# Performance work log

Hardware: AMD Instinct MI355X
Metric: run time of the kernel (lower is better)

The kernel has to match this reference:

```python
import jax, jax.numpy as jnp
import numpy as np

N_NODES = 50000
N_EDGES = 800000
N_GRAPHS = 512
F_IN = 128
D = 256
EPS = 1e-5
NEG_SLOPE = 0.01  # torch LeakyReLU default


def leaky_relu(x):
    return jnp.where(x >= 0, x, NEG_SLOPE * x)


def egnn_conv(x, edge_index, edge_attr, lin2_w, lin2_b, lin_w, lin_b, n_nodes):
    # message: LeakyReLU(lin(x_j + lin2(edge_attr))), aggregate: add at target i
    src, dst = edge_index[0], edge_index[1]
    ea = edge_attr @ lin2_w.T + lin2_b          # [E, in]
    msg = (x[src] + ea) @ lin_w.T + lin_b        # [E, out]
    msg = leaky_relu(msg)
    return jax.ops.segment_sum(msg, dst, num_segments=n_nodes)


def batch_norm(x, w, b):
    # training-mode BatchNorm1d: biased batch statistics over node axis
    mean = jnp.mean(x, axis=0)
    var = jnp.mean(jnp.square(x - mean), axis=0)
    return (x - mean) * jax.lax.rsqrt(var + EPS) * w + b


def setup_inputs() -> dict:
    key = jax.random.key(0)
    ks = jax.random.split(key, 8)
    inp = {
        "node_ids": jax.random.randint(ks[0], (N_NODES,), 0, 51),
        "edge_index": jax.random.randint(ks[1], (2, N_EDGES), 0, N_NODES),
        "edge_attr": jax.random.normal(ks[2], (N_EDGES, 4), dtype=jnp.float32),
        "batch": jnp.sort(jax.random.randint(ks[3], (N_NODES,), 0, N_GRAPHS)),
        "emb_table": jax.random.normal(ks[4], (51, F_IN), dtype=jnp.float32) * 0.1,
        "c1_lin2_w": jax.random.normal(ks[5], (F_IN, 4), dtype=jnp.float32) * 0.1,
        "c1_lin2_b": jnp.zeros((F_IN,), jnp.float32),
        "c1_lin_w": jax.random.normal(ks[6], (D, F_IN), dtype=jnp.float32) * (1.0 / np.sqrt(F_IN)),
        "c1_lin_b": jnp.zeros((D,), jnp.float32),
        "bn1_w": jnp.ones((D,), jnp.float32),
        "bn1_b": jnp.zeros((D,), jnp.float32),
        "c2_lin2_w": jax.random.normal(jax.random.fold_in(key, 10), (D, 4), dtype=jnp.float32) * 0.1,
        "c2_lin2_b": jnp.zeros((D,), jnp.float32),
        "c2_lin_w": jax.random.normal(ks[7], (D, D), dtype=jnp.float32) * (1.0 / np.sqrt(D)),
        "c2_lin_b": jnp.zeros((D,), jnp.float32),
        "bn2_w": jnp.ones((D,), jnp.float32),
        "bn2_b": jnp.zeros((D,), jnp.float32),
        "gate_w": jax.random.normal(jax.random.fold_in(key, 11), (1, D), dtype=jnp.float32) * 0.1,
        "gate_b": jnp.zeros((1,), jnp.float32),
    }
    return inp


def reference(node_ids, edge_index, edge_attr, batch, emb_table,
              c1_lin2_w, c1_lin2_b, c1_lin_w, c1_lin_b, bn1_w, bn1_b,
              c2_lin2_w, c2_lin2_b, c2_lin_w, c2_lin_b, bn2_w, bn2_b,
              gate_w, gate_b):
    x = emb_table[node_ids]                                   # [N, F_IN]
    x = egnn_conv(x, edge_index, edge_attr, c1_lin2_w, c1_lin2_b,
                  c1_lin_w, c1_lin_b, N_NODES)                # [N, D]
    x = leaky_relu(batch_norm(x, bn1_w, bn1_b))
    x2 = egnn_conv(x, edge_index, edge_attr, c2_lin2_w, c2_lin2_b,
                   c2_lin_w, c2_lin_b, N_NODES)               # [N, D]
    x2 = leaky_relu(batch_norm(x2, bn2_w, bn2_b))
    # AttentionalAggregation: softmax of gate over each graph segment
    gate = x2 @ gate_w.T + gate_b                             # [N, 1]
    gmax = jax.ops.segment_max(gate, batch, num_segments=N_GRAPHS)
    e = jnp.exp(gate - gmax[batch])                           # [N, 1]
    denom = jax.ops.segment_sum(e, batch, num_segments=N_GRAPHS)
    alpha = e / denom[batch]
    out = jax.ops.segment_sum(alpha * x2, batch, num_segments=N_GRAPHS)
    return out                                                # [G, D]
```

## Files before the change

kernel.cpp:

```cpp
#include <hip/hip_runtime.h>
#include <hip/hip_bf16.h>

#define NN 50000
#define NE 800000
#define NG 512

typedef __bf16 bf16_t;
typedef __bf16 bf16x8 __attribute__((ext_vector_type(8)));
typedef __bf16 bf16x4 __attribute__((ext_vector_type(4)));
typedef float f32x4 __attribute__((ext_vector_type(4)));
typedef float f32x2 __attribute__((ext_vector_type(2)));

__device__ __forceinline__ float lrelu(float v) { return v >= 0.f ? v : 0.01f * v; }

__device__ __forceinline__ f32x2 unpk2(unsigned w) {
    union { unsigned u; float f; } lo, hi;
    lo.u = w << 16;
    hi.u = w & 0xffff0000u;
    f32x2 r; r[0] = lo.f; r[1] = hi.f; return r;
}

__device__ __forceinline__ int vzero() {
    int vz;
    asm("v_mov_b32 %0, 0" : "=v"(vz));
    return vz;
}

__global__ void gme_setup(const float* __restrict__ emb,
                          const float* __restrict__ c1lw, const float* __restrict__ c1l2w,
                          const float* __restrict__ c1l2b, const float* __restrict__ c1lb,
                          const float* __restrict__ c2lw, const float* __restrict__ c2l2w,
                          const float* __restrict__ c2l2b, const float* __restrict__ c2lb,
                          bf16_t* __restrict__ TYB, float* __restrict__ WC1,
                          float* __restrict__ WC2, float* __restrict__ CB2,
                          bf16_t* __restrict__ W2B, int* __restrict__ CNT) {
    int b = blockIdx.x, t = threadIdx.x;
    if (b < 51) {
        const float4* er = (const float4*)(emb + b * 128);
        const float4* zb = (const float4*)c1l2b;
        const float4* wr = (const float4*)(c1lw + t * 128);
        float s = 0.f;
        for (int k = 0; k < 32; ++k) {
            float4 e = er[k], z = zb[k], w = wr[k];
            s += (e.x + z.x) * w.x + (e.y + z.y) * w.y + (e.z + z.z) * w.z + (e.w + z.w) * w.w;
        }
        TYB[b * 256 + t] = (bf16_t)(s + c1lb[t]);
    } else if (b == 51) {
        const float4* wr = (const float4*)(c1lw + t * 128);
        const float4* cw = (const float4*)c1l2w;
        float4 a = make_float4(0.f, 0.f, 0.f, 0.f);
        for (int k = 0; k < 32; ++k) {
            float4 w = wr[k];
            float4 c0 = cw[k * 4 + 0], c1 = cw[k * 4 + 1], c2 = cw[k * 4 + 2], c3 = cw[k * 4 + 3];
            a.x += w.x * c0.x + w.y * c1.x + w.z * c2.x + w.w * c3.x;
            a.y += w.x * c0.y + w.y * c1.y + w.z * c2.y + w.w * c3.y;
            a.z += w.x * c0.z + w.y * c1.z + w.z * c2.z + w.w * c3.z;
            a.w += w.x * c0.w + w.y * c1.w + w.z * c2.w + w.w * c3.w;
        }
        ((float4*)WC1)[t] = a;
    } else if (b == 52) {
        const float4* wr = (const float4*)(c2lw + t * 256);
        const float4* cw = (const float4*)c2l2w;
        const float4* zb = (const float4*)c2l2b;
        float4 a = make_float4(0.f, 0.f, 0.f, 0.f);
        float ab = 0.f;
        for (int k = 0; k < 64; ++k) {
            float4 w = wr[k];
            float4 c0 = cw[k * 4 + 0], c1 = cw[k * 4 + 1], c2 = cw[k * 4 + 2], c3 = cw[k * 4 + 3];
            float4 z = zb[k];
            a.x += w.x * c0.x + w.y * c1.x + w.z * c2.x + w.w * c3.x;
            a.y += w.x * c0.y + w.y * c1.y + w.z * c2.y + w.w * c3.y;
            a.z += w.x * c0.z + w.y * c1.z + w.z * c2.z + w.w * c3.z;
            a.w += w.x * c0.w + w.y * c1.w + w.z * c2.w + w.w * c3.w;
            ab += w.x * z.x + w.y * z.y + w.z * z.z + w.w * z.w;
        }
        ((float4*)WC2)[t] = a;
        CB2[t] = ab + c2lb[t];
    } else if (b < 117) {
        int i0 = (b - 53) * 1024;
        for (int r = 0; r < 4; ++r) {
            int i = i0 + r * 256 + t;
            W2B[i] = (bf16_t)c2lw[i];
        }
    } else {
        int i = (b - 117) * 256 + t;
        if (i < NN) CNT[i] = 0;
    }
}

__global__ void gme_count(const int* __restrict__ ei, int* __restrict__ cnt,
                          int* __restrict__ RK) {
    int e = blockIdx.x * 256 + threadIdx.x;
    if (e >= NE) return;
    RK[e] = atomicAdd(&cnt[ei[NE + e]], 1);
}

__global__ void gme_scan1(const int* __restrict__ CNT, int* __restrict__ LP,
                          int* __restrict__ BS) {
    __shared__ int lds[256];
    int b = blockIdx.x, t = threadIdx.x;
    int i = b * 196 + t;
    int v = (t < 196 && i < NN) ? CNT[i] : 0;
    lds[t] = v;
    __syncthreads();
    for (int off = 1; off < 256; off <<= 1) {
        int u = (t >= off) ? lds[t - off] : 0;
        __syncthreads();
        lds[t] += u;
        __syncthreads();
    }
    if (t < 196 && i < NN) LP[i] = lds[t] - v;
    if (t == 255) BS[b] = lds[255];
}

__global__ void gme_scan2(const int* __restrict__ BS, int* __restrict__ BX,
                          int* __restrict__ RS) {
    __shared__ int lds[256];
    int t = threadIdx.x;
    int v = BS[t];
    lds[t] = v;
    __syncthreads();
    for (int off = 1; off < 256; off <<= 1) {
        int u = (t >= off) ? lds[t - off] : 0;
        __syncthreads();
        lds[t] += u;
        __syncthreads();
    }
    BX[t] = lds[t] - v;
    if (t == 255) RS[NN] = lds[255];
}

__global__ void gme_scan3(const int* __restrict__ LP, const int* __restrict__ BX,
                          int* __restrict__ RS,
                          const int* __restrict__ batch, int* __restrict__ GS) {
    int b = blockIdx.x, t = threadIdx.x;
    if (t >= 196) return;
    int i = b * 196 + t;
    if (i >= NN) return;
    RS[i] = BX[b] + LP[i];
    int bb = batch[i];
    if (i == 0) {
        for (int g = 0; g <= bb; ++g) GS[g] = 0;
    } else {
        int a = batch[i - 1];
        for (int g = a + 1; g <= bb; ++g) GS[g] = i;
    }
    if (i == NN - 1) {
        for (int g = bb + 1; g <= NG; ++g) GS[g] = NN;
    }
}

__global__ void gme_scatter(const int* __restrict__ ei,
                            const float4* __restrict__ eattr,
                            const int* __restrict__ node_ids,
                            const int* __restrict__ RS, const int* __restrict__ RK,
                            uint4* __restrict__ SE) {
    int e = blockIdx.x * 256 + threadIdx.x;
    if (e >= NE) return;
    int s = ei[e];
    int d = ei[NE + e];
    int nid = node_ids[s];
    float4 at = eattr[e];
    union { bf16_t h[2]; unsigned u; } p01, p23;
    p01.h[0] = (bf16_t)at.x; p01.h[1] = (bf16_t)at.y;
    p23.h[0] = (bf16_t)at.z; p23.h[1] = (bf16_t)at.w;
    int pos = RS[d] + RK[e];
    SE[pos] = make_uint4((unsigned)(s | (nid << 16)), p01.u, p23.u, 0u);
}

__global__ __launch_bounds__(256) void gme_conv0(
        const int* __restrict__ RS, const uint4* __restrict__ SE,
        const bf16_t* __restrict__ TYB, const float* __restrict__ Wc,
        float* __restrict__ agg, float* __restrict__ PARTS) {
    __shared__ __align__(16) uint2 sTY[51 * 64];
    {
        const uint4* s4 = (const uint4*)TYB;
        uint4* d4 = (uint4*)sTY;
        for (int i = threadIdx.x; i < 51 * 32; i += 256) d4[i] = s4[i];
    }
    __syncthreads();
    int lane = threadIdx.x & 63;
    int w = threadIdx.x >> 6;
    int vz = vzero();
    const float4* wc4 = (const float4*)Wc;
    int c4 = lane * 4;
    float4 w0 = wc4[c4 + 0], w1 = wc4[c4 + 1], w2 = wc4[c4 + 2], w3 = wc4[c4 + 3];
    f32x2 wA0 = {w0.x, w1.x}, wB0 = {w0.y, w1.y}, wC0 = {w0.z, w1.z}, wD0 = {w0.w, w1.w};
    f32x2 wA1 = {w2.x, w3.x}, wB1 = {w2.y, w3.y}, wC1 = {w2.z, w3.z}, wD1 = {w2.w, w3.w};
    const f32x2 zero = {0.f, 0.f};
    const uint2* lrow = sTY + lane;
    int base = blockIdx.x * 16 + w * 4;
    f32x2 ssum0 = zero, ssum1 = zero, qsum0 = zero, qsum1 = zero;
#pragma unroll 1
    for (int k = 0; k < 4; ++k) {
        int node = __builtin_amdgcn_readfirstlane(base + k);
        int rs = RS[node], re = RS[node + 1];
        f32x2 accP0 = zero, accP1 = zero, accA0 = zero, accA1 = zero;
        auto accum = [&](uint4 se, uint2 r) {
            f32x2 y0 = unpk2(r.x), y1 = unpk2(r.y);
            f32x2 axy = unpk2(se.y), azw = unpk2(se.z);
            f32x2 ax = {axy[0], axy[0]}, ay = {axy[1], axy[1]};
            f32x2 az = {azw[0], azw[0]}, aw = {azw[1], azw[1]};
            f32x2 m0 = __builtin_elementwise_fma(ax, wA0, y0);
            f32x2 m1 = __builtin_elementwise_fma(ax, wA1, y1);
            m0 = __builtin_elementwise_fma(ay, wB0, m0);
            m1 = __builtin_elementwise_fma(ay, wB1, m1);
            m0 = __builtin_elementwise_fma(az, wC0, m0);
            m1 = __builtin_elementwise_fma(az, wC1, m1);
            m0 = __builtin_elementwise_fma(aw, wD0, m0);
            m1 = __builtin_elementwise_fma(aw, wD1, m1);
            accA0 += m0; accA1 += m1;
            accP0 += __builtin_elementwise_max(m0, zero);
            accP1 += __builtin_elementwise_max(m1, zero);
        };
        int j = rs;
        for (; j + 8 <= re; j += 8) {
            uint4 se[8]; uint2 r[8];
#pragma unroll
            for (int u = 0; u < 8; ++u) se[u] = SE[j + u + vz];
#pragma unroll
            for (int u = 0; u < 8; ++u) r[u] = lrow[(se[u].x >> 16) << 6];
#pragma unroll
            for (int u = 0; u < 8; ++u) accum(se[u], r[u]);
        }
        if (j + 4 <= re) {
            uint4 se[4]; uint2 r[4];
#pragma unroll
            for (int u = 0; u < 4; ++u) se[u] = SE[j + u + vz];
#pragma unroll
            for (int u = 0; u < 4; ++u) r[u] = lrow[(se[u].x >> 16) << 6];
#pragma unroll
            for (int u = 0; u < 4; ++u) accum(se[u], r[u]);
            j += 4;
        }
        for (; j < re; ++j) {
            uint4 se = SE[j + vz];
            accum(se, lrow[(se.x >> 16) << 6]);
        }
        const f32x2 c99 = {0.99f, 0.99f}, c01 = {0.01f, 0.01f};
        f32x2 o0 = __builtin_elementwise_fma(accP0, c99, accA0 * c01);
        f32x2 o1 = __builtin_elementwise_fma(accP1, c99, accA1 * c01);
        *((float4*)(agg + node * 256) + lane) = make_float4(o0[0], o0[1], o1[0], o1[1]);
        ssum0 += o0; ssum1 += o1;
        qsum0 += o0 * o0; qsum1 += o1 * o1;
    }
    __syncthreads();
    float* red = (float*)sTY;
    red[w * 512 + c4 + 0] = ssum0[0]; red[w * 512 + c4 + 1] = ssum0[1];
    red[w * 512 + c4 + 2] = ssum1[0]; red[w * 512 + c4 + 3] = ssum1[1];
    red[w * 512 + 256 + c4 + 0] = qsum0[0]; red[w * 512 + 256 + c4 + 1] = qsum0[1];
    red[w * 512 + 256 + c4 + 2] = qsum1[0]; red[w * 512 + 256 + c4 + 3] = qsum1[1];
    __syncthreads();
    int cc = threadIdx.x;
    float s = red[cc] + red[512 + cc] + red[1024 + cc] + red[1536 + cc];
    float q = red[256 + cc] + red[768 + cc] + red[1280 + cc] + red[1792 + cc];
    int prow = (blockIdx.x & 255) * 512;
    atomicAdd(&PARTS[prow + cc], s);
    atomicAdd(&PARTS[prow + 256 + cc], q);
}

__global__ __launch_bounds__(256, 4) void gme_conv1(
        const int* __restrict__ RS, const uint4* __restrict__ SE,
        const bf16_t* __restrict__ QB, const float* __restrict__ Wc,
        float* __restrict__ agg, float* __restrict__ PARTS) {
    __shared__ float red[2048];
    int lane = threadIdx.x & 63;
    int w = threadIdx.x >> 6;
    int node = __builtin_amdgcn_readfirstlane(blockIdx.x * 4 + w);
    const float4* wc4 = (const float4*)Wc;
    int c4 = lane * 4;
    float4 w0 = wc4[c4 + 0], w1 = wc4[c4 + 1], w2 = wc4[c4 + 2], w3 = wc4[c4 + 3];
    f32x2 wA0 = {w0.x, w1.x}, wB0 = {w0.y, w1.y}, wC0 = {w0.z, w1.z}, wD0 = {w0.w, w1.w};
    f32x2 wA1 = {w2.x, w3.x}, wB1 = {w2.y, w3.y}, wC1 = {w2.z, w3.z}, wD1 = {w2.w, w3.w};
    const f32x2 zero = {0.f, 0.f};
    f32x2 accP0 = zero, accP1 = zero, accA0 = zero, accA1 = zero;
    int rs = RS[node], re = RS[node + 1];
    const char* yb = (const char*)QB;
    unsigned loff = (unsigned)(lane << 3);
    auto rowld = [&](unsigned row) -> uint2 {
        return *(const uint2*)(yb + (row << 9) + loff);
    };
    auto accum = [&](uint4 se, uint2 r) {
        f32x2 y0 = unpk2(r.x), y1 = unpk2(r.y);
        f32x2 axy = unpk2(se.y), azw = unpk2(se.z);
        f32x2 ax = {axy[0], axy[0]}, ay = {axy[1], axy[1]};
        f32x2 az = {azw[0], azw[0]}, aw = {azw[1], azw[1]};
        f32x2 m0 = __builtin_elementwise_fma(ax, wA0, y0);
        f32x2 m1 = __builtin_elementwise_fma(ax, wA1, y1);
        m0 = __builtin_elementwise_fma(ay, wB0, m0);
        m1 = __builtin_elementwise_fma(ay, wB1, m1);
        m0 = __builtin_elementwise_fma(az, wC0, m0);
        m1 = __builtin_elementwise_fma(az, wC1, m1);
        m0 = __builtin_elementwise_fma(aw, wD0, m0);
        m1 = __builtin_elementwise_fma(aw, wD1, m1);
        accA0 += m0; accA1 += m1;
        accP0 += __builtin_elementwise_max(m0, zero);
        accP1 += __builtin_elementwise_max(m1, zero);
    };
    int j = rs;
    if (j + 8 <= re) {
        uint4 se[8];
#pragma unroll
        for (int u = 0; u < 8; ++u) se[u] = SE[j + u];
        while (true) {
            uint2 r[8];
#pragma unroll
            for (int u = 0; u < 8; ++u) r[u] = rowld(se[u].x & 0xffffu);
            bool more = (j + 16 <= re);
            uint4 seN[8];
            if (more) {
#pragma unroll
                for (int u = 0; u < 8; ++u) seN[u] = SE[j + 8 + u];
            }
#pragma unroll
            for (int u = 0; u < 8; ++u) accum(se[u], r[u]);
            j += 8;
            if (!more) break;
#pragma unroll
            for (int u = 0; u < 8; ++u) se[u] = seN[u];
        }
    }
    if (j + 4 <= re) {
        uint4 se[4]; uint2 r[4];
#pragma unroll
        for (int u = 0; u < 4; ++u) se[u] = SE[j + u];
#pragma unroll
        for (int u = 0; u < 4; ++u) r[u] = rowld(se[u].x & 0xffffu);
#pragma unroll
        for (int u = 0; u < 4; ++u) accum(se[u], r[u]);
        j += 4;
    }
    for (; j < re; ++j) {
        uint4 se = SE[j];
        accum(se, rowld(se.x & 0xffffu));
    }
    const f32x2 c99 = {0.99f, 0.99f}, c01 = {0.01f, 0.01f};
    f32x2 o0 = __builtin_elementwise_fma(accP0, c99, accA0 * c01);
    f32x2 o1 = __builtin_elementwise_fma(accP1, c99, accA1 * c01);
    *((float4*)(agg + node * 256) + lane) = make_float4(o0[0], o0[1], o1[0], o1[1]);
    red[w * 512 + c4 + 0] = o0[0]; red[w * 512 + c4 + 1] = o0[1];
    red[w * 512 + c4 + 2] = o1[0]; red[w * 512 + c4 + 3] = o1[1];
    red[w * 512 + 256 + c4 + 0] = o0[0] * o0[0];
    red[w * 512 + 256 + c4 + 1] = o0[1] * o0[1];
    red[w * 512 + 256 + c4 + 2] = o1[0] * o1[0];
    red[w * 512 + 256 + c4 + 3] = o1[1] * o1[1];
    __syncthreads();
    int cc = threadIdx.x;
    float s = red[cc] + red[512 + cc] + red[1024 + cc] + red[1536 + cc];
    float q = red[256 + cc] + red[768 + cc] + red[1280 + cc] + red[1792 + cc];
    int prow = (blockIdx.x & 255) * 512;
    atomicAdd(&PARTS[prow + cc], s);
    atomicAdd(&PARTS[prow + 256 + cc], q);
}

__global__ __launch_bounds__(512) void gme_bred(float* __restrict__ PARTS,
                                                float* __restrict__ ST, int zero) {
    int t = threadIdx.x;
    int b = blockIdx.x;
    float acc = 0.f;
#pragma unroll
    for (int r = 0; r < 16; ++r) acc += PARTS[(b * 16 + r) * 512 + t];
    atomicAdd(&ST[t], acc);
    if (zero) {
#pragma unroll
        for (int r = 0; r < 16; ++r) PARTS[(b * 16 + r) * 512 + t] = 0.f;
    }
}

__global__ __launch_bounds__(256) void gme_gemm(const float* __restrict__ P,
                                                const float* __restrict__ ST,
                                                const float* __restrict__ bw,
                                                const float* __restrict__ bb,
                                                const bf16_t* __restrict__ W2B,
                                                const float* __restrict__ CB2,
                                                bf16_t* __restrict__ QB) {
    __shared__ float s_sc[256], s_sh[256];
    __shared__ __align__(16) uint4 sB[8192];
    {
        int c = threadIdx.x;
        float mean = ST[c] * (1.f / NN);
        float var = ST[256 + c] * (1.f / NN) - mean * mean;
        float sc = bw[c] * rsqrtf(var + 1e-5f);
        s_sc[c] = sc;
        s_sh[c] = bb[c] - mean * sc;
        const uint4* w4 = (const uint4*)W2B;
#pragma unroll
        for (int it = 0; it < 32; ++it) {
            int i = it * 256 + c;
            int row = i >> 5, slot = i & 31;
            sB[(row << 5) | (slot ^ (row & 7))] = w4[i];
        }
    }
    __syncthreads();
    int lane = threadIdx.x & 63;
    int wave = blockIdx.x * 4 + (threadIdx.x >> 6);
    if (wave >= NN / 16) return;
    int m0 = wave * 16;
    int r = lane & 15, q = lane >> 4;
    int rx = r & 7;
    const float* arow = P + (m0 + r) * 256 + q * 8;
    bf16x8 a[8];
#pragma unroll
    for (int kt = 0; kt < 8; ++kt) {
        int k0 = kt * 32 + q * 8;
        float4 u0 = *(const float4*)(arow + kt * 32);
        float4 u1 = *(const float4*)(arow + kt * 32 + 4);
        bf16x8 f;
        f[0] = (bf16_t)lrelu(fmaf(u0.x, s_sc[k0 + 0], s_sh[k0 + 0]));
        f[1] = (bf16_t)lrelu(fmaf(u0.y, s_sc[k0 + 1], s_sh[k0 + 1]));
        f[2] = (bf16_t)lrelu(fmaf(u0.z, s_sc[k0 + 2], s_sh[k0 + 2]));
        f[3] = (bf16_t)lrelu(fmaf(u0.w, s_sc[k0 + 3], s_sh[k0 + 3]));
        f[4] = (bf16_t)lrelu(fmaf(u1.x, s_sc[k0 + 4], s_sh[k0 + 4]));
        f[5] = (bf16_t)lrelu(fmaf(u1.y, s_sc[k0 + 5], s_sh[k0 + 5]));
        f[6] = (bf16_t)lrelu(fmaf(u1.z, s_sc[k0 + 6], s_sh[k0 + 6]));
        f[7] = (bf16_t)lrelu(fmaf(u1.w, s_sc[k0 + 7], s_sh[k0 + 7]));
        a[kt] = f;
    }
#pragma unroll 1
    for (int g = 0; g < 2; ++g) {
        f32x4 acc[8];
#pragma unroll
        for (int n8 = 0; n8 < 8; ++n8) acc[n8] = (f32x4){0.f, 0.f, 0.f, 0.f};
#pragma unroll
        for (int kt = 0; kt < 8; ++kt) {
            int slot = (kt * 4 + q) ^ rx;
            bf16x8 bf[8];
#pragma unroll
            for (int n8 = 0; n8 < 8; ++n8) {
                int row = g * 128 + n8 * 16 + r;
                bf[n8] = *(const bf16x8*)&sB[(row << 5) | slot];
            }
#pragma unroll
            for (int n8 = 0; n8 < 8; ++n8) {
                acc[n8] = __builtin_amdgcn_mfma_f32_16x16x32_bf16(bf[n8], a[kt], acc[n8], 0, 0, 0);
            }
        }
#pragma unroll
        for (int n8 = 0; n8 < 8; ++n8) {
            int nt = g * 8 + n8;
            float4 cbv = ((const float4*)CB2)[nt * 4 + q];
            bf16x4 o;
            o[0] = (bf16_t)(acc[n8][0] + cbv.x);
            o[1] = (bf16_t)(acc[n8][1] + cbv.y);
            o[2] = (bf16_t)(acc[n8][2] + cbv.z);
            o[3] = (bf16_t)(acc[n8][3] + cbv.w);
            *(bf16x4*)(QB + (m0 + r) * 256 + nt * 16 + q * 4) = o;
        }
    }
}

__global__ __launch_bounds__(256) void gme_attn(const int* __restrict__ GS,
                                                const float* __restrict__ P,
                                                const float* __restrict__ ST,
                                                const float* __restrict__ bw,
                                                const float* __restrict__ bb,
                                                const float* __restrict__ gw,
                                                const float* __restrict__ gb,
                                                float* __restrict__ out) {
    __shared__ float gl[1024];
    __shared__ float rr[8];
    int g = blockIdx.x, t = threadIdx.x;
    int lo = GS[g], hi = GS[g + 1];
    if (lo >= hi) { out[g * 256 + t] = 0.f; return; }
    int lane = t & 63, w = t >> 6;
    {
        float4 s4 = ((const float4*)ST)[lane];
        float4 q4 = ((const float4*)(ST + 256))[lane];
        float4 w4 = ((const float4*)bw)[lane];
        float4 b4 = ((const float4*)bb)[lane];
        float4 g4 = ((const float4*)gw)[lane];
        float m0 = s4.x * (1.f / NN), m1 = s4.y * (1.f / NN);
        float m2 = s4.z * (1.f / NN), m3 = s4.w * (1.f / NN);
        float sc0 = w4.x * rsqrtf(q4.x * (1.f / NN) - m0 * m0 + 1e-5f);
        float sc1 = w4.y * rsqrtf(q4.y * (1.f / NN) - m1 * m1 + 1e-5f);
        float sc2 = w4.z * rsqrtf(q4.z * (1.f / NN) - m2 * m2 + 1e-5f);
        float sc3 = w4.w * rsqrtf(q4.w * (1.f / NN) - m3 * m3 + 1e-5f);
        float sh0 = b4.x - m0 * sc0, sh1 = b4.y - m1 * sc1;
        float sh2 = b4.z - m2 * sc2, sh3 = b4.w - m3 * sc3;
        float gb0 = gb[0];
        for (int n = lo + w; n < hi; n += 4) {
            float4 p = *(const float4*)(P + n * 256 + lane * 4);
            float d = lrelu(fmaf(p.x, sc0, sh0)) * g4.x
                    + lrelu(fmaf(p.y, sc1, sh1)) * g4.y
                    + lrelu(fmaf(p.z, sc2, sh2)) * g4.z
                    + lrelu(fmaf(p.w, sc3, sh3)) * g4.w;
#pragma unroll
            for (int off = 32; off > 0; off >>= 1) d += __shfl_xor(d, off, 64);
            if (lane == 0) gl[n - lo] = d + gb0;
        }
    }
    __syncthreads();
    int cnt = hi - lo;
    float lm = -3.0e38f;
    for (int i = t; i < cnt; i += 256) lm = fmaxf(lm, gl[i]);
#pragma unroll
    for (int off = 32; off > 0; off >>= 1) lm = fmaxf(lm, __shfl_xor(lm, off, 64));
    if (lane == 0) rr[w] = lm;
    __syncthreads();
    float mx = fmaxf(fmaxf(rr[0], rr[1]), fmaxf(rr[2], rr[3]));
    float ls = 0.f;
    for (int i = t; i < cnt; i += 256) { float e = expf(gl[i] - mx); gl[i] = e; ls += e; }
#pragma unroll
    for (int off = 32; off > 0; off >>= 1) ls += __shfl_xor(ls, off, 64);
    if (lane == 0) rr[4 + w] = ls;
    __syncthreads();
    float sinv = 1.f / (rr[4] + rr[5] + rr[6] + rr[7]);
    float mean = ST[t] * (1.f / NN);
    float var = ST[256 + t] * (1.f / NN) - mean * mean;
    float sc = bw[t] * rsqrtf(var + 1e-5f);
    float sh = bb[t] - mean * sc;
    float a0 = 0.f, a1 = 0.f, a2 = 0.f, a3 = 0.f;
    int n = lo;
    for (; n + 4 <= hi; n += 4) {
        float p0 = P[n * 256 + t], p1 = P[(n + 1) * 256 + t];
        float p2 = P[(n + 2) * 256 + t], p3 = P[(n + 3) * 256 + t];
        a0 = fmaf(gl[n - lo + 0], lrelu(fmaf(p0, sc, sh)), a0);
        a1 = fmaf(gl[n - lo + 1], lrelu(fmaf(p1, sc, sh)), a1);
        a2 = fmaf(gl[n - lo + 2], lrelu(fmaf(p2, sc, sh)), a2);
        a3 = fmaf(gl[n - lo + 3], lrelu(fmaf(p3, sc, sh)), a3);
    }
    for (; n < hi; ++n) a0 = fmaf(gl[n - lo], lrelu(fmaf(P[n * 256 + t], sc, sh)), a0);
    out[g * 256 + t] = (a0 + a1 + a2 + a3) * sinv;
}

extern "C" void kernel_launch(void* const* d_in, const int* in_sizes, int n_in,
                              void* d_out, int out_size, void* d_ws, size_t ws_size,
                              hipStream_t stream) {
    const int* node_ids = (const int*)d_in[0];
    const int* edge_index = (const int*)d_in[1];
    const float4* edge_attr = (const float4*)d_in[2];
    const int* batch = (const int*)d_in[3];
    const float* emb = (const float*)d_in[4];
    const float* c1l2w = (const float*)d_in[5];
    const float* c1l2b = (const float*)d_in[6];
    const float* c1lw = (const float*)d_in[7];
    const float* c1lb = (const float*)d_in[8];
    const float* bn1w = (const float*)d_in[9];
    const float* bn1b = (const float*)d_in[10];
    const float* c2l2w = (const float*)d_in[11];
    const float* c2l2b = (const float*)d_in[12];
    const float* c2lw = (const float*)d_in[13];
    const float* c2lb = (const float*)d_in[14];
    const float* bn2w = (const float*)d_in[15];
    const float* bn2b = (const float*)d_in[16];
    const float* gate_w = (const float*)d_in[17];
    const float* gate_b = (const float*)d_in[18];

    char* ws = (char*)d_ws;
    size_t oP = 0;
    size_t oQB = oP + 51200000;
    size_t oSE = oQB + 25600000;
    size_t oRK = oSE + 12800000;
    size_t oRS = oRK + 3200000;
    size_t oCNT = oRS + 200064;
    size_t oLP = oCNT + 200000;
    size_t oBS = oLP + 200000;
    size_t oBX = oBS + 1024;
    size_t oTY = oBX + 1024;
    size_t oWC1 = oTY + 52224;
    size_t oWC2 = oWC1 + 4096;
    size_t oCB2 = oWC2 + 4096;
    size_t oW2B = oCB2 + 1024;
    size_t oST = oW2B + 131072;
    size_t oPARTS = oST + 4096;
    size_t oGS = oPARTS + 524288;

    float* P = (float*)(ws + oP);
    bf16_t* QB = (bf16_t*)(ws + oQB);
    uint4* SE = (uint4*)(ws + oSE);
    int* RK = (int*)(ws + oRK);
    int* RS = (int*)(ws + oRS);
    int* CNT = (int*)(ws + oCNT);
    int* LP = (int*)(ws + oLP);
    int* BS = (int*)(ws + oBS);
    int* BX = (int*)(ws + oBX);
    bf16_t* TYB = (bf16_t*)(ws + oTY);
    float* WC1 = (float*)(ws + oWC1);
    float* WC2 = (float*)(ws + oWC2);
    float* CB2 = (float*)(ws + oCB2);
    bf16_t* W2B = (bf16_t*)(ws + oW2B);
    float* ST1 = (float*)(ws + oST);
    float* ST2 = ST1 + 512;
    float* PARTS = (float*)(ws + oPARTS);
    int* GS = (int*)(ws + oGS);

    hipMemsetAsync(ST1, 0, 4096 + 524288, stream);

    gme_setup<<<313, 256, 0, stream>>>(emb, c1lw, c1l2w, c1l2b, c1lb,
                                       c2lw, c2l2w, c2l2b, c2lb,
                                       TYB, WC1, WC2, CB2, W2B, CNT);
    gme_count<<<NE / 256, 256, 0, stream>>>(edge_index, CNT, RK);
    gme_scan1<<<256, 256, 0, stream>>>(CNT, LP, BS);
    gme_scan2<<<1, 256, 0, stream>>>(BS, BX, RS);
    gme_scan3<<<256, 256, 0, stream>>>(LP, BX, RS, batch, GS);
    gme_scatter<<<NE / 256, 256, 0, stream>>>(edge_index, edge_attr, node_ids,
                                              RS, RK, SE);
    gme_conv0<<<NN / 16, 256, 0, stream>>>(RS, SE, TYB, WC1, P, PARTS);
    gme_bred<<<16, 512, 0, stream>>>(PARTS, ST1, 1);
    gme_gemm<<<(NN / 16 + 3) / 4, 256, 0, stream>>>(P, ST1, bn1w, bn1b, W2B, CB2, QB);
    gme_conv1<<<NN / 4, 256, 0, stream>>>(RS, SE, QB, WC2, P, PARTS);
    gme_bred<<<16, 512, 0, stream>>>(PARTS, ST2, 0);
    gme_attn<<<NG, 256, 0, stream>>>(GS, P, ST2, bn2w, bn2b, gate_w, gate_b,
                                     (float*)d_out);
}
```

Baseline: 363.6 us.

## Store conv aggregates in bf16 and software-pipeline edge loads in conv0

The per-node aggregate buffer P written by both conv kernels is now stored as bf16 instead of fp32, and the gemm and attention kernels read and unpack bf16. This halves the traffic of the 50000x256 intermediate on write and on its subsequent reads. Batch-norm statistics are still accumulated from the fp32 values, but the normalized inputs now carry bf16 rounding. Separately, the conv0 edge loop prefetches the next 8 edge records while accumulating the current 8, to hide global load latency at the cost of extra registers.

```diff
diff --git a/kernel.cpp b/kernel.cpp
--- a/kernel.cpp
+++ b/kernel.cpp
@@ -18,6 +18,12 @@
     lo.u = w << 16;
     hi.u = w & 0xffff0000u;
     f32x2 r; r[0] = lo.f; r[1] = hi.f; return r;
+}
+
+__device__ __forceinline__ unsigned pk2(float a, float b) {
+    union { bf16_t h[2]; unsigned u; } p;
+    p.h[0] = (bf16_t)a; p.h[1] = (bf16_t)b;
+    return p.u;
 }
 
 __device__ __forceinline__ int vzero() {
@@ -161,17 +167,14 @@
     int d = ei[NE + e];
     int nid = node_ids[s];
     float4 at = eattr[e];
-    union { bf16_t h[2]; unsigned u; } p01, p23;
-    p01.h[0] = (bf16_t)at.x; p01.h[1] = (bf16_t)at.y;
-    p23.h[0] = (bf16_t)at.z; p23.h[1] = (bf16_t)at.w;
     int pos = RS[d] + RK[e];
-    SE[pos] = make_uint4((unsigned)(s | (nid << 16)), p01.u, p23.u, 0u);
+    SE[pos] = make_uint4((unsigned)(s | (nid << 16)), pk2(at.x, at.y), pk2(at.z, at.w), 0u);
 }
 
 __global__ __launch_bounds__(256) void gme_conv0(
         const int* __restrict__ RS, const uint4* __restrict__ SE,
         const bf16_t* __restrict__ TYB, const float* __restrict__ Wc,
-        float* __restrict__ agg, float* __restrict__ PARTS) {
+        bf16_t* __restrict__ agg, float* __restrict__ PARTS) {
     __shared__ __align__(16) uint2 sTY[51 * 64];
     {
         const uint4* s4 = (const uint4*)TYB;
@@ -214,14 +217,27 @@
             accP1 += __builtin_elementwise_max(m1, zero);
         };
         int j = rs;
-        for (; j + 8 <= re; j += 8) {
-            uint4 se[8]; uint2 r[8];
+        if (j + 8 <= re) {
+            uint4 se[8];
 #pragma unroll
             for (int u = 0; u < 8; ++u) se[u] = SE[j + u + vz];
-#pragma unroll
-            for (int u = 0; u < 8; ++u) r[u] = lrow[(se[u].x >> 16) << 6];
-#pragma unroll
-            for (int u = 0; u < 8; ++u) accum(se[u], r[u]);
+            while (true) {
+                uint2 r[8];
+#pragma unroll
+                for (int u = 0; u < 8; ++u) r[u] = lrow[(se[u].x >> 16) << 6];
+                bool more = (j + 16 <= re);
+                uint4 seN[8];
+                if (more) {
+#pragma unroll
+                    for (int u = 0; u < 8; ++u) seN[u] = SE[j + 8 + u + vz];
+                }
+#pragma unroll
+                for (int u = 0; u < 8; ++u) accum(se[u], r[u]);
+                j += 8;
+                if (!more) break;
+#pragma unroll
+                for (int u = 0; u < 8; ++u) se[u] = seN[u];
+            }
         }
         if (j + 4 <= re) {
             uint4 se[4]; uint2 r[4];
@@ -240,7 +256,10 @@
         const f32x2 c99 = {0.99f, 0.99f}, c01 = {0.01f, 0.01f};
         f32x2 o0 = __builtin_elementwise_fma(accP0, c99, accA0 * c01);
         f32x2 o1 = __builtin_elementwise_fma(accP1, c99, accA1 * c01);
-        *((float4*)(agg + node * 256) + lane) = make_float4(o0[0], o0[1], o1[0], o1[1]);
+        uint2 ov;
+        ov.x = pk2(o0[0], o0[1]);
+        ov.y = pk2(o1[0], o1[1]);
+        *((uint2*)(agg + node * 256) + lane) = ov;
         ssum0 += o0; ssum1 += o1;
         qsum0 += o0 * o0; qsum1 += o1 * o1;
     }
@@ -262,7 +281,7 @@
 __global__ __launch_bounds__(256, 4) void gme_conv1(
         const int* __restrict__ RS, const uint4* __restrict__ SE,
         const bf16_t* __restrict__ QB, const float* __restrict__ Wc,
-        float* __restrict__ agg, float* __restrict__ PARTS) {
+        bf16_t* __restrict__ agg, float* __restrict__ PARTS) {
     __shared__ float red[2048];
     int lane = threadIdx.x & 63;
     int w = threadIdx.x >> 6;
@@ -337,7 +356,10 @@
     const f32x2 c99 = {0.99f, 0.99f}, c01 = {0.01f, 0.01f};
     f32x2 o0 = __builtin_elementwise_fma(accP0, c99, accA0 * c01);
     f32x2 o1 = __builtin_elementwise_fma(accP1, c99, accA1 * c01);
-    *((float4*)(agg + node * 256) + lane) = make_float4(o0[0], o0[1], o1[0], o1[1]);
+    uint2 ov;
+    ov.x = pk2(o0[0], o0[1]);
+    ov.y = pk2(o1[0], o1[1]);
+    *((uint2*)(agg + node * 256) + lane) = ov;
     red[w * 512 + c4 + 0] = o0[0]; red[w * 512 + c4 + 1] = o0[1];
     red[w * 512 + c4 + 2] = o1[0]; red[w * 512 + c4 + 3] = o1[1];
     red[w * 512 + 256 + c4 + 0] = o0[0] * o0[0];
@@ -367,7 +389,7 @@
     }
 }
 
-__global__ __launch_bounds__(256) void gme_gemm(const float* __restrict__ P,
+__global__ __launch_bounds__(256) void gme_gemm(const bf16_t* __restrict__ P,
                                                 const float* __restrict__ ST,
                                                 const float* __restrict__ bw,
                                                 const float* __restrict__ bb,
@@ -398,22 +420,22 @@
     int m0 = wave * 16;
     int r = lane & 15, q = lane >> 4;
     int rx = r & 7;
-    const float* arow = P + (m0 + r) * 256 + q * 8;
+    const uint4* arow = (const uint4*)(P + (m0 + r) * 256);
     bf16x8 a[8];
 #pragma unroll
     for (int kt = 0; kt < 8; ++kt) {
         int k0 = kt * 32 + q * 8;
-        float4 u0 = *(const float4*)(arow + kt * 32);
-        float4 u1 = *(const float4*)(arow + kt * 32 + 4);
+        uint4 u = arow[q + kt * 4];
+        f32x2 v0 = unpk2(u.x), v1 = unpk2(u.y), v2 = unpk2(u.z), v3 = unpk2(u.w);
         bf16x8 f;
-        f[0] = (bf16_t)lrelu(fmaf(u0.x, s_sc[k0 + 0], s_sh[k0 + 0]));
-        f[1] = (bf16_t)lrelu(fmaf(u0.y, s_sc[k0 + 1], s_sh[k0 + 1]));
-        f[2] = (bf16_t)lrelu(fmaf(u0.z, s_sc[k0 + 2], s_sh[k0 + 2]));
-        f[3] = (bf16_t)lrelu(fmaf(u0.w, s_sc[k0 + 3], s_sh[k0 + 3]));
-        f[4] = (bf16_t)lrelu(fmaf(u1.x, s_sc[k0 + 4], s_sh[k0 + 4]));
-        f[5] = (bf16_t)lrelu(fmaf(u1.y, s_sc[k0 + 5], s_sh[k0 + 5]));
-        f[6] = (bf16_t)lrelu(fmaf(u1.z, s_sc[k0 + 6], s_sh[k0 + 6]));
-        f[7] = (bf16_t)lrelu(fmaf(u1.w, s_sc[k0 + 7], s_sh[k0 + 7]));
+        f[0] = (bf16_t)lrelu(fmaf(v0[0], s_sc[k0 + 0], s_sh[k0 + 0]));
+        f[1] = (bf16_t)lrelu(fmaf(v0[1], s_sc[k0 + 1], s_sh[k0 + 1]));
+        f[2] = (bf16_t)lrelu(fmaf(v1[0], s_sc[k0 + 2], s_sh[k0 + 2]));
+        f[3] = (bf16_t)lrelu(fmaf(v1[1], s_sc[k0 + 3], s_sh[k0 + 3]));
+        f[4] = (bf16_t)lrelu(fmaf(v2[0], s_sc[k0 + 4], s_sh[k0 + 4]));
+        f[5] = (bf16_t)lrelu(fmaf(v2[1], s_sc[k0 + 5], s_sh[k0 + 5]));
+        f[6] = (bf16_t)lrelu(fmaf(v3[0], s_sc[k0 + 6], s_sh[k0 + 6]));
+        f[7] = (bf16_t)lrelu(fmaf(v3[1], s_sc[k0 + 7], s_sh[k0 + 7]));
         a[kt] = f;
     }
 #pragma unroll 1
@@ -450,7 +472,7 @@
 }
 
 __global__ __launch_bounds__(256) void gme_attn(const int* __restrict__ GS,
-                                                const float* __restrict__ P,
+                                                const bf16_t* __restrict__ P,
                                                 const float* __restrict__ ST,
                                                 const float* __restrict__ bw,
                                                 const float* __restrict__ bb,
@@ -479,11 +501,12 @@
         float sh2 = b4.z - m2 * sc2, sh3 = b4.w - m3 * sc3;
         float gb0 = gb[0];
         for (int n = lo + w; n < hi; n += 4) {
-            float4 p = *(const float4*)(P + n * 256 + lane * 4);
-            float d = lrelu(fmaf(p.x, sc0, sh0)) * g4.x
-                    + lrelu(fmaf(p.y, sc1, sh1)) * g4.y
-                    + lrelu(fmaf(p.z, sc2, sh2)) * g4.z
-                    + lrelu(fmaf(p.w, sc3, sh3)) * g4.w;
+            uint2 u = *((const uint2*)(P + n * 256) + lane);
+            f32x2 p01 = unpk2(u.x), p23 = unpk2(u.y);
+            float d = lrelu(fmaf(p01[0], sc0, sh0)) * g4.x
+                    + lrelu(fmaf(p01[1], sc1, sh1)) * g4.y
+                    + lrelu(fmaf(p23[0], sc2, sh2)) * g4.z
+                    + lrelu(fmaf(p23[1], sc3, sh3)) * g4.w;
 #pragma unroll
             for (int off = 32; off > 0; off >>= 1) d += __shfl_xor(d, off, 64);
             if (lane == 0) gl[n - lo] = d + gb0;
@@ -512,14 +535,14 @@
     float a0 = 0.f, a1 = 0.f, a2 = 0.f, a3 = 0.f;
     int n = lo;
     for (; n + 4 <= hi; n += 4) {
-        float p0 = P[n * 256 + t], p1 = P[(n + 1) * 256 + t];
-        float p2 = P[(n + 2) * 256 + t], p3 = P[(n + 3) * 256 + t];
+        float p0 = (float)P[n * 256 + t], p1 = (float)P[(n + 1) * 256 + t];
+        float p2 = (float)P[(n + 2) * 256 + t], p3 = (float)P[(n + 3) * 256 + t];
         a0 = fmaf(gl[n - lo + 0], lrelu(fmaf(p0, sc, sh)), a0);
         a1 = fmaf(gl[n - lo + 1], lrelu(fmaf(p1, sc, sh)), a1);
         a2 = fmaf(gl[n - lo + 2], lrelu(fmaf(p2, sc, sh)), a2);
         a3 = fmaf(gl[n - lo + 3], lrelu(fmaf(p3, sc, sh)), a3);
     }
-    for (; n < hi; ++n) a0 = fmaf(gl[n - lo], lrelu(fmaf(P[n * 256 + t], sc, sh)), a0);
+    for (; n < hi; ++n) a0 = fmaf(gl[n - lo], lrelu(fmaf((float)P[n * 256 + t], sc, sh)), a0);
     out[g * 256 + t] = (a0 + a1 + a2 + a3) * sinv;
 }
 
@@ -548,7 +571,7 @@
 
     char* ws = (char*)d_ws;
     size_t oP = 0;
-    size_t oQB = oP + 51200000;
+    size_t oQB = oP + 25600000;
     size_t oSE = oQB + 25600000;
     size_t oRK = oSE + 12800000;
     size_t oRS = oRK + 3200000;
@@ -565,7 +588,7 @@
     size_t oPARTS = oST + 4096;
     size_t oGS = oPARTS + 524288;
 
-    float* P = (float*)(ws + oP);
+    bf16_t* P = (bf16_t*)(ws + oP);
     bf16_t* QB = (bf16_t*)(ws + oQB);
     uint4* SE = (uint4*)(ws + oSE);
     int* RK = (int*)(ws + oRK);
```

After: 355.4 us. 1.02x faster.
